# Performance work log

Hardware: AMD Instinct MI355X
Metric: run time of the kernel (lower is better)

## Reference

```python
import jax, jax.numpy as jnp
import numpy as np

B, S, H, HD = 2, 2048, 16, 128
HID = H * HD            # 2048
FF = 4 * HID            # 8192
ROT = int(HD * 0.25)    # 32 rotary dims (rotary_pct=0.25)
EPS = 1e-5
ROPE_BASE = 10000.0


def _layernorm(x, g, b):
    mu = jnp.mean(x, axis=-1, keepdims=True)
    var = jnp.mean(jnp.square(x - mu), axis=-1, keepdims=True)
    return (x - mu) * jax.lax.rsqrt(var + EPS) * g + b


def _rope_cos_sin(seq_len, dim, dtype):
    inv_freq = 1.0 / (ROPE_BASE ** (np.arange(0, dim, 2, dtype=np.float32) / dim))
    t = np.arange(seq_len, dtype=np.float32)
    freqs = np.outer(t, inv_freq)              # [S, dim/2]
    emb = np.concatenate([freqs, freqs], -1)   # [S, dim]
    return jnp.asarray(np.cos(emb), dtype), jnp.asarray(np.sin(emb), dtype)


def _apply_rope(x, cos, sin):
    # x: [B, H, S, ROT]; GPTNeoX rotate_half
    half = x.shape[-1] // 2
    x1, x2 = x[..., :half], x[..., half:]
    rot = jnp.concatenate([-x2, x1], axis=-1)
    return x * cos[None, None, :, :] + rot * sin[None, None, :, :]


def setup_inputs() -> dict:
    key = jax.random.key(0)
    ks = jax.random.split(key, 8)
    f = jnp.float32
    return {
        "hidden_states": jax.random.normal(ks[0], (B, S, HID), f),
        "ln1_g": jnp.ones((HID,), f), "ln1_b": jnp.zeros((HID,), f),
        "ln2_g": jnp.ones((HID,), f), "ln2_b": jnp.zeros((HID,), f),
        "W_qkv": jax.random.normal(ks[1], (HID, 3 * HID), f) * 0.02,
        "b_qkv": jnp.zeros((3 * HID,), f),
        "W_o": jax.random.normal(ks[2], (HID, HID), f) * 0.02,
        "b_o": jnp.zeros((HID,), f),
        "W_fc": jax.random.normal(ks[3], (HID, FF), f) * 0.02,
        "b_fc": jnp.zeros((FF,), f),
        "W_proj": jax.random.normal(ks[4], (FF, HID), f) * 0.02,
        "b_proj": jnp.zeros((HID,), f),
    }


def reference(hidden_states, ln1_g, ln1_b, ln2_g, ln2_b,
              W_qkv, b_qkv, W_o, b_o, W_fc, b_fc, W_proj, b_proj):
    dtype = hidden_states.dtype
    x = _layernorm(hidden_states, ln1_g, ln1_b)

    # fused QKV, GPTNeoX per-head interleaved layout [B,S,H,3*HD]
    qkv = (x @ W_qkv + b_qkv).reshape(B, S, H, 3 * HD)
    q = jnp.transpose(qkv[..., :HD], (0, 2, 1, 3))          # [B,H,S,HD]
    k = jnp.transpose(qkv[..., HD:2 * HD], (0, 2, 1, 3))
    v = jnp.transpose(qkv[..., 2 * HD:], (0, 2, 1, 3))

    cos, sin = _rope_cos_sin(S, ROT, dtype)
    q = jnp.concatenate([_apply_rope(q[..., :ROT], cos, sin), q[..., ROT:]], -1)
    k = jnp.concatenate([_apply_rope(k[..., :ROT], cos, sin), k[..., ROT:]], -1)

    # eager attention: scores / sqrt(hd), causal mask-fill, softmax, matmul
    scale = 1.0 / jnp.sqrt(jnp.asarray(HD, dtype))
    scores = jnp.einsum("bhqd,bhkd->bhqk", q, k) * scale
    causal = jnp.tril(jnp.ones((S, S), bool))
    scores = jnp.where(causal, scores, jnp.finfo(dtype).min)
    weights = jax.nn.softmax(scores, axis=-1)
    ctx = jnp.einsum("bhqk,bhkd->bhqd", weights, v)          # [B,H,S,HD]
    ctx = jnp.transpose(ctx, (0, 2, 1, 3)).reshape(B, S, HID)
    attn_out = ctx @ W_o + b_o

    # parallel residual: mlp(ln2(h)) + attn(ln1(h)) + h
    m = _layernorm(hidden_states, ln2_g, ln2_b)
    mlp_out = jax.nn.gelu(m @ W_fc + b_fc, approximate=False) @ W_proj + b_proj
    return mlp_out + attn_out + hidden_states
```

## Files before the change

### kernel.cpp

```cpp
#include <hip/hip_runtime.h>
#include <hip/hip_bf16.h>
#include <math.h>

#define BDIM 2
#define SDIM 2048
#define HDIM 16
#define HD 128
#define HID 2048
#define FFD 8192
#define NTOK (BDIM*SDIM)
#define QKVW (3*HID)

typedef __hip_bfloat16 bf16;
typedef __attribute__((ext_vector_type(8))) short short8;
typedef __attribute__((ext_vector_type(4))) short short4_;
typedef __attribute__((ext_vector_type(4))) float floatx4;

__device__ inline short bfbits(float f) {
  bf16 h = __float2bfloat16(f);
  short s;
  __builtin_memcpy(&s, &h, 2);
  return s;
}

__global__ __launch_bounds__(256) void transpose_cvt(
    const float* __restrict__ W, bf16* __restrict__ Wt, int K, int N)
{
  __shared__ float tile[32][33];
  int n0 = blockIdx.x * 32, k0 = blockIdx.y * 32;
  int tx = threadIdx.x, ty = threadIdx.y;
  #pragma unroll
  for (int r = ty; r < 32; r += 8)
    tile[r][tx] = W[(size_t)(k0 + r) * N + n0 + tx];
  __syncthreads();
  #pragma unroll
  for (int r = ty; r < 32; r += 8)
    Wt[(size_t)(n0 + r) * K + k0 + tx] = __float2bfloat16(tile[tx][r]);
}

__global__ __launch_bounds__(256) void ln_both(
    const float* __restrict__ x,
    const float* __restrict__ g1, const float* __restrict__ b1,
    const float* __restrict__ g2, const float* __restrict__ b2,
    bf16* __restrict__ o1, bf16* __restrict__ o2)
{
  int row = blockIdx.x;
  int tid = threadIdx.x;
  const float4* xr = (const float4*)(x + (size_t)row * HID);
  float4 va = xr[tid], vb = xr[tid + 256];
  float s = va.x + va.y + va.z + va.w + vb.x + vb.y + vb.z + vb.w;
  float q = va.x*va.x + va.y*va.y + va.z*va.z + va.w*va.w
          + vb.x*vb.x + vb.y*vb.y + vb.z*vb.z + vb.w*vb.w;
  #pragma unroll
  for (int off = 1; off < 64; off <<= 1) {
    s += __shfl_xor(s, off);
    q += __shfl_xor(q, off);
  }
  __shared__ float red[8];
  int wave = tid >> 6;
  if ((tid & 63) == 0) { red[wave] = s; red[4 + wave] = q; }
  __syncthreads();
  s = red[0] + red[1] + red[2] + red[3];
  q = red[4] + red[5] + red[6] + red[7];
  float mu = s * (1.0f / HID);
  float var = q * (1.0f / HID) - mu * mu;
  float rs = rsqrtf(var + 1e-5f);

  const float4* g1v = (const float4*)g1; const float4* b1v = (const float4*)b1;
  const float4* g2v = (const float4*)g2; const float4* b2v = (const float4*)b2;
  short4_* o1v = (short4_*)(o1 + (size_t)row * HID);
  short4_* o2v = (short4_*)(o2 + (size_t)row * HID);
  #pragma unroll
  for (int p = 0; p < 2; ++p) {
    int e = tid + p * 256;
    float4 xv = (p == 0) ? va : vb;
    float4 gv = g1v[e], bv = b1v[e];
    short4_ pk;
    pk[0] = bfbits((xv.x - mu) * rs * gv.x + bv.x);
    pk[1] = bfbits((xv.y - mu) * rs * gv.y + bv.y);
    pk[2] = bfbits((xv.z - mu) * rs * gv.z + bv.z);
    pk[3] = bfbits((xv.w - mu) * rs * gv.w + bv.w);
    o1v[e] = pk;
    gv = g2v[e]; bv = b2v[e];
    pk[0] = bfbits((xv.x - mu) * rs * gv.x + bv.x);
    pk[1] = bfbits((xv.y - mu) * rs * gv.y + bv.y);
    pk[2] = bfbits((xv.z - mu) * rs * gv.z + bv.z);
    pk[3] = bfbits((xv.w - mu) * rs * gv.w + bv.w);
    o2v[e] = pk;
  }
}

template<int EPI>
__global__ __launch_bounds__(256) void gemm_bt(
    const bf16* __restrict__ A, const bf16* __restrict__ Bt,
    const float* __restrict__ bias,
    float* __restrict__ Cf, bf16* __restrict__ Cb,
    const bf16* __restrict__ r1b, const float* __restrict__ r2,
    int M, int N, int K)
{
  __shared__ bf16 As[128 * 32];
  __shared__ bf16 Bs[128 * 32];
  const int tid = threadIdx.x;
  const int wave = tid >> 6, lane = tid & 63;
  const int quad = lane >> 4, l16 = lane & 15;
  const int n0 = blockIdx.x * 128, m0 = blockIdx.y * 128;
  const int wm = (wave >> 1) * 64, wn = (wave & 1) * 64;
  const int lrow = lane >> 2, lcol = (lane & 3) * 8;

  floatx4 acc[4][4];
  #pragma unroll
  for (int i = 0; i < 4; ++i)
    #pragma unroll
    for (int j = 0; j < 4; ++j) acc[i][j] = (floatx4)0.0f;

  const int KT = K >> 5;
  for (int kt = 0; kt < KT; ++kt) {
    #pragma unroll
    for (int t = 0; t < 2; ++t) {
      int c = wave * 2 + t;
      const bf16* ga = A + (size_t)(m0 + c * 16 + lrow) * K + kt * 32 + lcol;
      const bf16* gb = Bt + (size_t)(n0 + c * 16 + lrow) * K + kt * 32 + lcol;
      __builtin_amdgcn_global_load_lds(
          (const __attribute__((address_space(1))) void*)ga,
          (__attribute__((address_space(3))) void*)&As[c * 512], 16, 0, 0);
      __builtin_amdgcn_global_load_lds(
          (const __attribute__((address_space(1))) void*)gb,
          (__attribute__((address_space(3))) void*)&Bs[c * 512], 16, 0, 0);
    }
    __syncthreads();
    short8 av[4], bv[4];
    #pragma unroll
    for (int i = 0; i < 4; ++i)
      av[i] = *(const short8*)&As[(wm + i * 16 + l16) * 32 + quad * 8];
    #pragma unroll
    for (int j = 0; j < 4; ++j)
      bv[j] = *(const short8*)&Bs[(wn + j * 16 + l16) * 32 + quad * 8];
    #pragma unroll
    for (int i = 0; i < 4; ++i)
      #pragma unroll
      for (int j = 0; j < 4; ++j)
        acc[i][j] = __builtin_amdgcn_mfma_f32_16x16x32_bf16(av[i], bv[j], acc[i][j], 0, 0, 0);
    __syncthreads();
  }

  #pragma unroll
  for (int i = 0; i < 4; ++i) {
    #pragma unroll
    for (int j = 0; j < 4; ++j) {
      int col = n0 + wn + j * 16 + l16;
      float bsv = bias[col];
      #pragma unroll
      for (int r = 0; r < 4; ++r) {
        int row = m0 + wm + i * 16 + quad * 4 + r;
        size_t idx = (size_t)row * N + col;
        float v = acc[i][j][r] + bsv;
        if (EPI == 1) {
          v = 0.5f * v * (1.0f + erff(v * 0.70710678118654752f));
          Cb[idx] = __float2bfloat16(v);
        } else if (EPI == 2) {
          Cf[idx] = v + __bfloat162float(r1b[idx]) + r2[idx];
        } else {
          Cb[idx] = __float2bfloat16(v);
        }
      }
    }
  }
}

__global__ __launch_bounds__(256) void rope_vt(
    bf16* __restrict__ qkv, bf16* __restrict__ vT)
{
  int bh = blockIdx.x, s0 = blockIdx.y * 32;
  int b = bh >> 4, h = bh & 15;
  int tid = threadIdx.x;
  __shared__ bf16 vs[32][136];

  for (int idx = tid; idx < 512; idx += 256) {
    int sl = idx >> 4, d = idx & 15;
    int s = s0 + sl;
    bf16* base = qkv + (size_t)(b * SDIM + s) * QKVW + h * 384;
    float fr = (float)s * expf(-(float)d * 0.5756462732485114f);
    float c = cosf(fr), sn = sinf(fr);
    float q1 = __bfloat162float(base[d]);
    float q2 = __bfloat162float(base[d + 16]);
    float k1 = __bfloat162float(base[128 + d]);
    float k2 = __bfloat162float(base[128 + d + 16]);
    base[d]        = __float2bfloat16(q1 * c - q2 * sn);
    base[d + 16]   = __float2bfloat16(q2 * c + q1 * sn);
    base[128 + d]      = __float2bfloat16(k1 * c - k2 * sn);
    base[128 + d + 16] = __float2bfloat16(k2 * c + k1 * sn);
  }

  for (int idx = tid; idx < 32 * 128; idx += 256) {
    int sl = idx >> 7, d = idx & 127;
    vs[sl][d] = qkv[(size_t)(b * SDIM + s0 + sl) * QKVW + h * 384 + 256 + d];
  }
  __syncthreads();
  for (int idx = tid; idx < 32 * 128; idx += 256) {
    int d = idx >> 5, sl = idx & 31;
    vT[((size_t)bh * HD + d) * SDIM + s0 + sl] = vs[sl][d];
  }
}

__global__ __launch_bounds__(256) void flash_attn(
    const bf16* __restrict__ qkv, const bf16* __restrict__ vT,
    bf16* __restrict__ ctx)
{
  int bh = blockIdx.x;
  int qb = gridDim.y - 1 - blockIdx.y;
  int b = bh >> 4, h = bh & 15;
  int tid = threadIdx.x;
  int wave = tid >> 6, lane = tid & 63;
  int quad = lane >> 4, l16 = lane & 15;
  int q0 = qb * 64 + wave * 16;
  const bf16* Qb = qkv + (size_t)b * SDIM * QKVW + h * 384;
  const bf16* Kb = Qb + 128;
  const bf16* Vb = vT + (size_t)bh * HD * SDIM;
  __shared__ bf16 Ps[4][16][32];

  short8 aq[4];
  #pragma unroll
  for (int c = 0; c < 4; ++c)
    aq[c] = *(const short8*)&Qb[(size_t)(q0 + l16) * QKVW + c * 32 + quad * 8];

  floatx4 o[8];
  #pragma unroll
  for (int d = 0; d < 8; ++d) o[d] = (floatx4)0.0f;
  float m_run[4] = {-INFINITY, -INFINITY, -INFINITY, -INFINITY};
  float l_run[4] = {0.0f, 0.0f, 0.0f, 0.0f};
  const float scale = 0.08838834764831845f;

  int tmax = (q0 + 15) >> 5;
  for (int t = 0; t <= tmax; ++t) {
    int k0 = t * 32;
    floatx4 sc[2];
    sc[0] = (floatx4)0.0f; sc[1] = (floatx4)0.0f;
    #pragma unroll
    for (int nh = 0; nh < 2; ++nh) {
      const bf16* kp = &Kb[(size_t)(k0 + nh * 16 + l16) * QKVW + quad * 8];
      #pragma unroll
      for (int c = 0; c < 4; ++c) {
        short8 kb = *(const short8*)&kp[c * 32];
        sc[nh] = __builtin_amdgcn_mfma_f32_16x16x32_bf16(aq[c], kb, sc[nh], 0, 0, 0);
      }
    }
    #pragma unroll
    for (int nh = 0; nh < 2; ++nh) {
      int col = k0 + nh * 16 + l16;
      #pragma unroll
      for (int r = 0; r < 4; ++r) {
        int row = q0 + quad * 4 + r;
        float v = sc[nh][r] * scale;
        sc[nh][r] = (col <= row) ? v : -1e30f;
      }
    }
    float alpha[4];
    #pragma unroll
    for (int r = 0; r < 4; ++r) {
      float mx = fmaxf(sc[0][r], sc[1][r]);
      mx = fmaxf(mx, __shfl_xor(mx, 1));
      mx = fmaxf(mx, __shfl_xor(mx, 2));
      mx = fmaxf(mx, __shfl_xor(mx, 4));
      mx = fmaxf(mx, __shfl_xor(mx, 8));
      float mnew = fmaxf(m_run[r], mx);
      alpha[r] = __expf(m_run[r] - mnew);
      m_run[r] = mnew;
      sc[0][r] = __expf(sc[0][r] - mnew);
      sc[1][r] = __expf(sc[1][r] - mnew);
      float sm = sc[0][r] + sc[1][r];
      sm += __shfl_xor(sm, 1);
      sm += __shfl_xor(sm, 2);
      sm += __shfl_xor(sm, 4);
      sm += __shfl_xor(sm, 8);
      l_run[r] = l_run[r] * alpha[r] + sm;
    }
    #pragma unroll
    for (int d = 0; d < 8; ++d) {
      o[d][0] *= alpha[0]; o[d][1] *= alpha[1];
      o[d][2] *= alpha[2]; o[d][3] *= alpha[3];
    }
    #pragma unroll
    for (int nh = 0; nh < 2; ++nh)
      #pragma unroll
      for (int r = 0; r < 4; ++r)
        Ps[wave][quad * 4 + r][nh * 16 + l16] = __float2bfloat16(sc[nh][r]);
    short8 pf = *(const short8*)&Ps[wave][l16][quad * 8];
    #pragma unroll
    for (int d = 0; d < 8; ++d) {
      short8 vb = *(const short8*)&Vb[(size_t)(d * 16 + l16) * SDIM + k0 + quad * 8];
      o[d] = __builtin_amdgcn_mfma_f32_16x16x32_bf16(pf, vb, o[d], 0, 0, 0);
    }
  }

  #pragma unroll
  for (int d = 0; d < 8; ++d) {
    #pragma unroll
    for (int r = 0; r < 4; ++r) {
      int row = q0 + quad * 4 + r;
      size_t tok = (size_t)b * SDIM + row;
      ctx[tok * HID + h * HD + d * 16 + l16] = __float2bfloat16(o[d][r] / l_run[r]);
    }
  }
}

extern "C" void kernel_launch(void* const* d_in, const int* in_sizes, int n_in,
                              void* d_out, int out_size, void* d_ws, size_t ws_size,
                              hipStream_t stream) {
  const float* hidden = (const float*)d_in[0];
  const float* ln1g = (const float*)d_in[1];
  const float* ln1b = (const float*)d_in[2];
  const float* ln2g = (const float*)d_in[3];
  const float* ln2b = (const float*)d_in[4];
  const float* Wqkv = (const float*)d_in[5];
  const float* bqkv = (const float*)d_in[6];
  const float* Wo   = (const float*)d_in[7];
  const float* bo   = (const float*)d_in[8];
  const float* Wfc  = (const float*)d_in[9];
  const float* bfc  = (const float*)d_in[10];
  const float* Wproj= (const float*)d_in[11];
  const float* bproj= (const float*)d_in[12];

  char* ws = (char*)d_ws;
  const size_t SZ_WQKV = (size_t)QKVW * HID * 2;
  const size_t SZ_WO   = (size_t)HID * HID * 2;
  const size_t SZ_WFC  = (size_t)FFD * HID * 2;
  const size_t SZ_WPROJ= (size_t)HID * FFD * 2;
  const size_t SZ_ACT  = (size_t)NTOK * HID * 2;
  const size_t SZ_QKV  = (size_t)NTOK * QKVW * 2;

  bf16* wqkvT = (bf16*)(ws + 0);
  bf16* woT   = (bf16*)(ws + SZ_WQKV);
  bf16* wfcT  = (bf16*)(ws + SZ_WQKV + SZ_WO);
  bf16* wprojT= (bf16*)(ws + SZ_WQKV + SZ_WO + SZ_WFC);
  char* actbase = ws + SZ_WQKV + SZ_WO + SZ_WFC + SZ_WPROJ;
  bf16* xln   = (bf16*)(actbase);
  bf16* mln   = (bf16*)(actbase + SZ_ACT);
  bf16* qkvb  = (bf16*)(actbase + 2 * SZ_ACT);
  bf16* vT    = (bf16*)(actbase + 2 * SZ_ACT + SZ_QKV);
  bf16* ctx   = xln;
  bf16* attnb = wqkvT;
  bf16* hfc   = qkvb;

  dim3 tblk(32, 8);
  transpose_cvt<<<dim3(QKVW / 32, HID / 32), tblk, 0, stream>>>(Wqkv, wqkvT, HID, QKVW);
  transpose_cvt<<<dim3(HID / 32, HID / 32), tblk, 0, stream>>>(Wo, woT, HID, HID);
  transpose_cvt<<<dim3(FFD / 32, HID / 32), tblk, 0, stream>>>(Wfc, wfcT, HID, FFD);
  transpose_cvt<<<dim3(HID / 32, FFD / 32), tblk, 0, stream>>>(Wproj, wprojT, FFD, HID);

  ln_both<<<NTOK, 256, 0, stream>>>(hidden, ln1g, ln1b, ln2g, ln2b, xln, mln);

  gemm_bt<3><<<dim3(48, 32), 256, 0, stream>>>(xln, wqkvT, bqkv, nullptr, qkvb,
                                               nullptr, nullptr, NTOK, QKVW, HID);

  rope_vt<<<dim3(32, SDIM / 32), 256, 0, stream>>>(qkvb, vT);

  flash_attn<<<dim3(32, SDIM / 64), 256, 0, stream>>>(qkvb, vT, ctx);

  gemm_bt<3><<<dim3(16, 32), 256, 0, stream>>>(ctx, woT, bo, nullptr, attnb,
                                               nullptr, nullptr, NTOK, HID, HID);

  gemm_bt<1><<<dim3(64, 32), 256, 0, stream>>>(mln, wfcT, bfc, nullptr, hfc,
                                               nullptr, nullptr, NTOK, FFD, HID);

  gemm_bt<2><<<dim3(16, 32), 256, 0, stream>>>(hfc, wprojT, bproj, (float*)d_out, nullptr,
                                               attnb, hidden, NTOK, HID, FFD);
}
```

Baseline: 1.149 ms.

## Pair causal query tiles per wave and prefetch K in flash attention

```diff
diff --git a/kernel.cpp b/kernel.cpp
--- a/kernel.cpp
+++ b/kernel.cpp
@@ -174,6 +174,7 @@
   int b = bh >> 4, h = bh & 15;
   int tid = threadIdx.x;
   __shared__ bf16 vs[32][136];
+  const float qsc = 0.12751740f;
 
   for (int idx = tid; idx < 512; idx += 256) {
     int sl = idx >> 4, d = idx & 15;
@@ -185,10 +186,15 @@
     float q2 = __bfloat162float(base[d + 16]);
     float k1 = __bfloat162float(base[128 + d]);
     float k2 = __bfloat162float(base[128 + d + 16]);
-    base[d]        = __float2bfloat16(q1 * c - q2 * sn);
-    base[d + 16]   = __float2bfloat16(q2 * c + q1 * sn);
+    base[d]        = __float2bfloat16(qsc * (q1 * c - q2 * sn));
+    base[d + 16]   = __float2bfloat16(qsc * (q2 * c + q1 * sn));
     base[128 + d]      = __float2bfloat16(k1 * c - k2 * sn);
     base[128 + d + 16] = __float2bfloat16(k2 * c + k1 * sn);
+  }
+  for (int idx = tid; idx < 32 * 96; idx += 256) {
+    int sl = idx / 96, d = 32 + idx % 96;
+    bf16* base = qkv + (size_t)(b * SDIM + s0 + sl) * QKVW + h * 384;
+    base[d] = __float2bfloat16(qsc * __bfloat162float(base[d]));
   }
 
   for (int idx = tid; idx < 32 * 128; idx += 256) {
@@ -202,103 +208,121 @@
   }
 }
 
+#define LOAD_K(KB, K0) { \
+  int krow_ = (K0); \
+  _Pragma("unroll") for (int nh_ = 0; nh_ < 2; ++nh_) \
+    _Pragma("unroll") for (int c_ = 0; c_ < 4; ++c_) \
+      KB[nh_*4+c_] = *(const short8*)&Kb[(size_t)(krow_ + nh_*16 + l16) * QKVW + c_*32 + quad*8]; }
+
+#define SOFTMAX(S0, S1, MR, LR, OO, ROWQ, DOMASK, K0, SLOT) { \
+  if (DOMASK) { \
+    _Pragma("unroll") for (int r_ = 0; r_ < 4; ++r_) { \
+      int row_ = (ROWQ) + quad*4 + r_; \
+      S0[r_] = ((K0) + l16 <= row_) ? S0[r_] : -1e30f; \
+      S1[r_] = ((K0) + 16 + l16 <= row_) ? S1[r_] : -1e30f; } } \
+  _Pragma("unroll") for (int r_ = 0; r_ < 4; ++r_) { \
+    float mx_ = fmaxf(S0[r_], S1[r_]); \
+    mx_ = fmaxf(mx_, __shfl_xor(mx_, 1)); \
+    mx_ = fmaxf(mx_, __shfl_xor(mx_, 2)); \
+    mx_ = fmaxf(mx_, __shfl_xor(mx_, 4)); \
+    mx_ = fmaxf(mx_, __shfl_xor(mx_, 8)); \
+    float mnew_ = fmaxf(MR[r_], mx_); \
+    float alpha_ = __builtin_amdgcn_exp2f(MR[r_] - mnew_); \
+    MR[r_] = mnew_; \
+    S0[r_] = __builtin_amdgcn_exp2f(S0[r_] - mnew_); \
+    S1[r_] = __builtin_amdgcn_exp2f(S1[r_] - mnew_); \
+    float sm_ = S0[r_] + S1[r_]; \
+    sm_ += __shfl_xor(sm_, 1); sm_ += __shfl_xor(sm_, 2); \
+    sm_ += __shfl_xor(sm_, 4); sm_ += __shfl_xor(sm_, 8); \
+    LR[r_] = LR[r_] * alpha_ + sm_; \
+    _Pragma("unroll") for (int d_ = 0; d_ < 8; ++d_) OO[d_][r_] *= alpha_; \
+    Ps[wave][SLOT][quad*4 + r_][l16]      = __float2bfloat16(S0[r_]); \
+    Ps[wave][SLOT][quad*4 + r_][16 + l16] = __float2bfloat16(S1[r_]); } }
+
+#define FLASH_ITER(IT, KC, KN) { \
+  const int k0_ = (IT) * 32; \
+  const int k0n_ = ((IT) + 1 < nk) ? k0_ + 32 : 0; \
+  LOAD_K(KN, k0n_); \
+  short8 vbuf_[8]; \
+  _Pragma("unroll") for (int d_ = 0; d_ < 8; ++d_) \
+    vbuf_[d_] = *(const short8*)&Vb[(size_t)(d_*16 + l16) * SDIM + k0_ + quad*8]; \
+  floatx4 scB_[2]; scB_[0] = (floatx4)0.0f; scB_[1] = (floatx4)0.0f; \
+  _Pragma("unroll") for (int c_ = 0; c_ < 4; ++c_) { \
+    scB_[0] = __builtin_amdgcn_mfma_f32_16x16x32_bf16(aqB[c_], KC[c_],   scB_[0], 0,0,0); \
+    scB_[1] = __builtin_amdgcn_mfma_f32_16x16x32_bf16(aqB[c_], KC[4+c_], scB_[1], 0,0,0); } \
+  const bool actA_ = (k0_ <= qa + 15); \
+  floatx4 scA_[2]; scA_[0] = (floatx4)0.0f; scA_[1] = (floatx4)0.0f; \
+  if (actA_) { \
+    _Pragma("unroll") for (int c_ = 0; c_ < 4; ++c_) { \
+      scA_[0] = __builtin_amdgcn_mfma_f32_16x16x32_bf16(aqA[c_], KC[c_],   scA_[0], 0,0,0); \
+      scA_[1] = __builtin_amdgcn_mfma_f32_16x16x32_bf16(aqA[c_], KC[4+c_], scA_[1], 0,0,0); } } \
+  SOFTMAX(scB_[0], scB_[1], mB, lB, oB, qb, (k0_ + 32 >= kmax), k0_, 0); \
+  if (actA_) { \
+    SOFTMAX(scA_[0], scA_[1], mA, lA, oA, qa, (k0_ + 32 > qa + 15), k0_, 1); \
+    short8 pfB_ = *(const short8*)&Ps[wave][0][l16][quad*8]; \
+    short8 pfA_ = *(const short8*)&Ps[wave][1][l16][quad*8]; \
+    _Pragma("unroll") for (int d_ = 0; d_ < 8; ++d_) { \
+      oB[d_] = __builtin_amdgcn_mfma_f32_16x16x32_bf16(pfB_, vbuf_[d_], oB[d_], 0,0,0); \
+      oA[d_] = __builtin_amdgcn_mfma_f32_16x16x32_bf16(pfA_, vbuf_[d_], oA[d_], 0,0,0); } \
+  } else { \
+    short8 pfB_ = *(const short8*)&Ps[wave][0][l16][quad*8]; \
+    _Pragma("unroll") for (int d_ = 0; d_ < 8; ++d_) \
+      oB[d_] = __builtin_amdgcn_mfma_f32_16x16x32_bf16(pfB_, vbuf_[d_], oB[d_], 0,0,0); } }
+
 __global__ __launch_bounds__(256) void flash_attn(
     const bf16* __restrict__ qkv, const bf16* __restrict__ vT,
     bf16* __restrict__ ctx)
 {
   int bh = blockIdx.x;
-  int qb = gridDim.y - 1 - blockIdx.y;
   int b = bh >> 4, h = bh & 15;
   int tid = threadIdx.x;
   int wave = tid >> 6, lane = tid & 63;
   int quad = lane >> 4, l16 = lane & 15;
-  int q0 = qb * 64 + wave * 16;
+  int p = blockIdx.y * 4 + wave;
+  int qa = 16 * p;
+  int qb = SDIM - 16 * (p + 1);
+  int kmax = qb + 16;
+  int nk = (kmax + 31) >> 5;
   const bf16* Qb = qkv + (size_t)b * SDIM * QKVW + h * 384;
   const bf16* Kb = Qb + 128;
   const bf16* Vb = vT + (size_t)bh * HD * SDIM;
-  __shared__ bf16 Ps[4][16][32];
-
-  short8 aq[4];
-  #pragma unroll
-  for (int c = 0; c < 4; ++c)
-    aq[c] = *(const short8*)&Qb[(size_t)(q0 + l16) * QKVW + c * 32 + quad * 8];
-
-  floatx4 o[8];
-  #pragma unroll
-  for (int d = 0; d < 8; ++d) o[d] = (floatx4)0.0f;
-  float m_run[4] = {-INFINITY, -INFINITY, -INFINITY, -INFINITY};
-  float l_run[4] = {0.0f, 0.0f, 0.0f, 0.0f};
-  const float scale = 0.08838834764831845f;
-
-  int tmax = (q0 + 15) >> 5;
-  for (int t = 0; t <= tmax; ++t) {
-    int k0 = t * 32;
-    floatx4 sc[2];
-    sc[0] = (floatx4)0.0f; sc[1] = (floatx4)0.0f;
-    #pragma unroll
-    for (int nh = 0; nh < 2; ++nh) {
-      const bf16* kp = &Kb[(size_t)(k0 + nh * 16 + l16) * QKVW + quad * 8];
-      #pragma unroll
-      for (int c = 0; c < 4; ++c) {
-        short8 kb = *(const short8*)&kp[c * 32];
-        sc[nh] = __builtin_amdgcn_mfma_f32_16x16x32_bf16(aq[c], kb, sc[nh], 0, 0, 0);
-      }
-    }
-    #pragma unroll
-    for (int nh = 0; nh < 2; ++nh) {
-      int col = k0 + nh * 16 + l16;
-      #pragma unroll
-      for (int r = 0; r < 4; ++r) {
-        int row = q0 + quad * 4 + r;
-        float v = sc[nh][r] * scale;
-        sc[nh][r] = (col <= row) ? v : -1e30f;
-      }
-    }
-    float alpha[4];
+  __shared__ bf16 Ps[4][2][16][32];
+
+  short8 aqA[4], aqB[4];
+  #pragma unroll
+  for (int c = 0; c < 4; ++c) {
+    aqA[c] = *(const short8*)&Qb[(size_t)(qa + l16) * QKVW + c * 32 + quad * 8];
+    aqB[c] = *(const short8*)&Qb[(size_t)(qb + l16) * QKVW + c * 32 + quad * 8];
+  }
+
+  floatx4 oA[8], oB[8];
+  #pragma unroll
+  for (int d = 0; d < 8; ++d) { oA[d] = (floatx4)0.0f; oB[d] = (floatx4)0.0f; }
+  float mA[4] = {-INFINITY, -INFINITY, -INFINITY, -INFINITY};
+  float mB[4] = {-INFINITY, -INFINITY, -INFINITY, -INFINITY};
+  float lA[4] = {0.0f, 0.0f, 0.0f, 0.0f};
+  float lB[4] = {0.0f, 0.0f, 0.0f, 0.0f};
+
+  short8 kb0[8], kb1[8];
+  LOAD_K(kb0, 0);
+  for (int it = 0; it < nk; it += 2) {
+    FLASH_ITER(it, kb0, kb1);
+    if (it + 1 < nk) { FLASH_ITER(it + 1, kb1, kb0); }
+  }
+
+  float rlA[4], rlB[4];
+  #pragma unroll
+  for (int r = 0; r < 4; ++r) { rlA[r] = 1.0f / lA[r]; rlB[r] = 1.0f / lB[r]; }
+  #pragma unroll
+  for (int d = 0; d < 8; ++d) {
     #pragma unroll
     for (int r = 0; r < 4; ++r) {
-      float mx = fmaxf(sc[0][r], sc[1][r]);
-      mx = fmaxf(mx, __shfl_xor(mx, 1));
-      mx = fmaxf(mx, __shfl_xor(mx, 2));
-      mx = fmaxf(mx, __shfl_xor(mx, 4));
-      mx = fmaxf(mx, __shfl_xor(mx, 8));
-      float mnew = fmaxf(m_run[r], mx);
-      alpha[r] = __expf(m_run[r] - mnew);
-      m_run[r] = mnew;
-      sc[0][r] = __expf(sc[0][r] - mnew);
-      sc[1][r] = __expf(sc[1][r] - mnew);
-      float sm = sc[0][r] + sc[1][r];
-      sm += __shfl_xor(sm, 1);
-      sm += __shfl_xor(sm, 2);
-      sm += __shfl_xor(sm, 4);
-      sm += __shfl_xor(sm, 8);
-      l_run[r] = l_run[r] * alpha[r] + sm;
-    }
-    #pragma unroll
-    for (int d = 0; d < 8; ++d) {
-      o[d][0] *= alpha[0]; o[d][1] *= alpha[1];
-      o[d][2] *= alpha[2]; o[d][3] *= alpha[3];
-    }
-    #pragma unroll
-    for (int nh = 0; nh < 2; ++nh)
-      #pragma unroll
-      for (int r = 0; r < 4; ++r)
-        Ps[wave][quad * 4 + r][nh * 16 + l16] = __float2bfloat16(sc[nh][r]);
-    short8 pf = *(const short8*)&Ps[wave][l16][quad * 8];
-    #pragma unroll
-    for (int d = 0; d < 8; ++d) {
-      short8 vb = *(const short8*)&Vb[(size_t)(d * 16 + l16) * SDIM + k0 + quad * 8];
-      o[d] = __builtin_amdgcn_mfma_f32_16x16x32_bf16(pf, vb, o[d], 0, 0, 0);
-    }
-  }
-
-  #pragma unroll
-  for (int d = 0; d < 8; ++d) {
-    #pragma unroll
-    for (int r = 0; r < 4; ++r) {
-      int row = q0 + quad * 4 + r;
-      size_t tok = (size_t)b * SDIM + row;
-      ctx[tok * HID + h * HD + d * 16 + l16] = __float2bfloat16(o[d][r] / l_run[r]);
+      int rowA = qa + quad * 4 + r;
+      int rowB = qb + quad * 4 + r;
+      ctx[((size_t)b * SDIM + rowA) * HID + h * HD + d * 16 + l16] =
+          __float2bfloat16(oA[d][r] * rlA[r]);
+      ctx[((size_t)b * SDIM + rowB) * HID + h * HD + d * 16 + l16] =
+          __float2bfloat16(oB[d][r] * rlB[r]);
     }
   }
 }
@@ -354,7 +378,7 @@
 
   rope_vt<<<dim3(32, SDIM / 32), 256, 0, stream>>>(qkvb, vT);
 
-  flash_attn<<<dim3(32, SDIM / 64), 256, 0, stream>>>(qkvb, vT, ctx);
+  flash_attn<<<dim3(32, SDIM / 128), 256, 0, stream>>>(qkvb, vT, ctx);
 
   gemm_bt<3><<<dim3(16, 32), 256, 0, stream>>>(ctx, woT, bo, nullptr, attnb,
                                                nullptr, nullptr, NTOK, HID, HID);
```

Result: faster. 1.100 ms (-4.2%).
